# Kernel optimization log

Hardware: AMD Instinct MI355X
Metric: run time of the kernel (lower is better)

## Reference

```python
import jax, jax.numpy as jnp
import numpy as np

EPS = 1e-5

def gather_neighbour(pc, idx):
    # pc: [B,N,d], idx: [B,Q,k] -> [B,Q,k,d]
    return jax.vmap(lambda p, i: p[i])(pc, idx)

def rel_pos_encoding(q_xyz, src_xyz, idx):
    # q_xyz: [B,Q,3], src_xyz: [B,N,3], idx: [B,Q,k] -> [B,Q,k,10]
    nbr = gather_neighbour(src_xyz, idx)              # [B,Q,k,3]
    tile = q_xyz[:, :, None, :]                       # [B,Q,1,3]
    rel = tile - nbr                                  # [B,Q,k,3]
    dis = jnp.sqrt(jnp.sum(rel * rel, axis=-1, keepdims=True))
    tile_b = jnp.broadcast_to(tile, nbr.shape)
    return jnp.concatenate([dis, rel, tile_b, nbr], axis=-1)

def conv_bn_relu(x, W, g, b, m, v):
    # 1x1 conv (bias-free) + inference BatchNorm + ReLU; x: [B,Q,K,Cin], W: [Cout,Cin]
    y = jnp.einsum('bqkc,oc->bqko', x, W)
    y = (y - m) * (g * jax.lax.rsqrt(v + EPS)) + b
    return jax.nn.relu(y)

def att_pool(x, Wfc, Wm, g, b, m, v):
    # x: [B,Q,K,C] -> [B,Q,1,Cout]; softmax over neighbor axis K
    att = jnp.einsum('bqkc,oc->bqko', x, Wfc)
    att = jax.nn.softmax(att, axis=2)
    agg = jnp.sum(x * att, axis=2, keepdims=True)     # [B,Q,1,C]
    return conv_bn_relu(agg, Wm, g, b, m, v)

def setup_inputs() -> dict:
    key = jax.random.key(0)
    ks = jax.random.split(key, 40)
    B, Q, k, Nd, Ns = 2, 16384, 16, 4096, 16384
    dim_lb, dim_sc, dim_nl = 128, 64, 128
    d_mid = dim_lb + 10 - dim_sc   # 74
    d_att = dim_lb + 10            # 138
    f32 = jnp.float32
    inp = {}
    inp['features_lb'] = jax.random.normal(ks[0], (B, Q, k, dim_lb), f32)
    inp['features_sc'] = jax.random.normal(ks[1], (B, Q, k, dim_sc), f32)
    inp['NM_lb'] = jax.random.randint(ks[2], (B, Q, k), 0, Nd)
    inp['NM_sc'] = jax.random.randint(ks[3], (B, Q, k), 0, Ns)
    inp['coords_lb'] = jax.random.normal(ks[4], (B, Nd, 3), f32)
    inp['coords_sc'] = jax.random.normal(ks[5], (B, Ns, 3), f32)
    inp['coords_queries'] = jax.random.normal(ks[6], (B, Q, 3), f32)
    inp['NM_cl'] = jax.random.randint(ks[7], (B, Q, k), 0, Q)
    def bn(i, c):
        return (jax.random.uniform(ks[i], (c,), f32) + 0.5,
                jax.random.normal(ks[i + 1], (c,), f32) * 0.1,
                jax.random.normal(ks[i + 2], (c,), f32) * 0.1,
                jax.random.uniform(ks[i + 3], (c,), f32) + 0.5)
    inp['W_lb'] = jax.random.normal(ks[8], (10, 10), f32) * 0.3
    inp['g_lb'], inp['b_lb'], inp['m_lb'], inp['v_lb'] = bn(9, 10)
    inp['W_sc'] = jax.random.normal(ks[13], (d_mid, 10), f32) * 0.3
    inp['g_sc'], inp['b_sc'], inp['m_sc'], inp['v_sc'] = bn(14, d_mid)
    inp['W_fc1'] = jax.random.normal(ks[18], (d_att, d_att), f32) * 0.08
    inp['W_mlp1'] = jax.random.normal(ks[19], (dim_nl, d_att), f32) * 0.08
    inp['g1'], inp['b1'], inp['m1'], inp['v1'] = bn(20, dim_nl)
    inp['W_cl'] = jax.random.normal(ks[24], (10, 10), f32) * 0.3
    inp['g_cl'], inp['b_cl'], inp['m_cl'], inp['v_cl'] = bn(25, 10)
    inp['W_fc2'] = jax.random.normal(ks[29], (d_att, d_att), f32) * 0.08
    inp['W_mlp2'] = jax.random.normal(ks[30], (dim_nl, d_att), f32) * 0.08
    inp['g2'], inp['b2'], inp['m2'], inp['v2'] = bn(31, dim_nl)
    return inp

def reference(features_lb, features_sc, NM_lb, NM_sc, coords_lb, coords_sc,
              coords_queries, NM_cl,
              W_lb, g_lb, b_lb, m_lb, v_lb,
              W_sc, g_sc, b_sc, m_sc, v_sc,
              W_fc1, W_mlp1, g1, b1, m1, v1,
              W_cl, g_cl, b_cl, m_cl, v_cl,
              W_fc2, W_mlp2, g2, b2, m2, v2):
    # branch 1: layer-below
    rppe_lb = conv_bn_relu(rel_pos_encoding(coords_queries, coords_lb, NM_lb),
                           W_lb, g_lb, b_lb, m_lb, v_lb)          # [B,Q,k,10]
    # branch 2: skip connection
    rppe_sc = conv_bn_relu(rel_pos_encoding(coords_queries, coords_sc, NM_sc),
                           W_sc, g_sc, b_sc, m_sc, v_sc)          # [B,Q,k,74]
    locSE_lb = jnp.concatenate([rppe_lb, features_lb], axis=-1)   # [B,Q,k,138]
    locSE_sc = jnp.concatenate([rppe_sc, features_sc], axis=-1)   # [B,Q,k,138]
    f_hat = jnp.concatenate([locSE_lb, locSE_sc], axis=2)         # [B,Q,2k,138]
    f_tilde = att_pool(f_hat, W_fc1, W_mlp1, g1, b1, m1, v1)      # [B,Q,1,128]
    # second aggregation over current layer (num_agg > 1)
    rppe_cl = conv_bn_relu(rel_pos_encoding(coords_queries, coords_queries, NM_cl),
                           W_cl, g_cl, b_cl, m_cl, v_cl)          # [B,Q,k,10]
    f_cur = gather_neighbour(f_tilde[:, :, 0, :], NM_cl)          # [B,Q,k,128]
    locSE_cl = jnp.concatenate([rppe_cl, f_cur], axis=-1)         # [B,Q,k,138]
    f_tilde = att_pool(locSE_cl, W_fc2, W_mlp2, g2, b2, m2, v2)   # [B,Q,1,128]
    # match torch output layout [B, dim_nl, Q, 1]
    return jnp.transpose(f_tilde, (0, 3, 1, 2))
```

## Files before the change

### kernel.cpp

```cpp
#include <hip/hip_runtime.h>
#include <cmath>

#define EPSF 1e-5f
typedef unsigned int  uint32;
typedef unsigned short u16;
typedef __attribute__((ext_vector_type(8))) short bfrag;
typedef __attribute__((ext_vector_type(4))) float f32x4;
typedef __attribute__((ext_vector_type(16))) float f32x16;

constexpr int Qn   = 16384;
constexpr int KS   = 168;
constexpr int PXS  = 42;
constexpr int AGS  = 168;
constexpr int Nd   = 4096;
constexpr float LOG2E = 1.4426950408889634f;

constexpr int OFF_W1  = 0;
constexpr int OFF_WM1 = 23040;
constexpr int OFF_W2  = 43520;
constexpr int OFF_WM2 = 66560;
constexpr int OFF_WLB = 87040;
constexpr int OFF_WSC = 87552;
constexpr int OFF_WCL = 90112;
constexpr int END_W   = 90624;
constexpr int BN_LB = 0;
constexpr int BN_SC = 20;
constexpr int BN_CL = 168;
constexpr int BN_M1 = 188;
constexpr int BN_M2 = 444;
constexpr int BN_TOT = 700;
constexpr int OFF_FT  = END_W + 2 * BN_TOT;
constexpr int OFF_AG  = OFF_FT + 2 * Qn * 128;
constexpr int OFF_W32 = OFF_AG + 2 * Qn * AGS;
constexpr int N_W32   = 2 * 5 * 10 * 512;
constexpr int PREP_N  = END_W + BN_TOT;

__device__ __forceinline__ u16 f2b(float f) {
    uint32 u = __float_as_uint(f);
    uint32 r = (u + 0x7fffu + ((u >> 16) & 1u)) >> 16;
    return (u16)r;
}
__device__ __forceinline__ float b2f(u16 h) {
    return __uint_as_float(((uint32)h) << 16);
}
__device__ __forceinline__ uint32 cvtpk(float a, float b) {
    uint32 r;
    asm("v_cvt_pk_bf16_f32 %0, %1, %2" : "=v"(r) : "v"(a), "v"(b));
    return r;
}
__device__ __forceinline__ u16 cvt1(float a) { return (u16)cvtpk(a, a); }
__device__ __forceinline__ float exp2_hw(float x) { return __builtin_amdgcn_exp2f(x); }

__global__ __launch_bounds__(256) void prep_weights(
    const float* __restrict__ Wfc1, const float* __restrict__ Wmlp1,
    const float* __restrict__ Wfc2, const float* __restrict__ Wmlp2,
    const float* __restrict__ Wlb,  const float* __restrict__ Wsc,
    const float* __restrict__ Wcl,
    const float* __restrict__ g_lb, const float* __restrict__ b_lb,
    const float* __restrict__ m_lb, const float* __restrict__ v_lb,
    const float* __restrict__ g_sc, const float* __restrict__ b_sc,
    const float* __restrict__ m_sc, const float* __restrict__ v_sc,
    const float* __restrict__ g_cl, const float* __restrict__ b_cl,
    const float* __restrict__ m_cl, const float* __restrict__ v_cl,
    const float* __restrict__ g1, const float* __restrict__ b1,
    const float* __restrict__ m1, const float* __restrict__ v1,
    const float* __restrict__ g2, const float* __restrict__ b2,
    const float* __restrict__ m2, const float* __restrict__ v2,
    u16* __restrict__ ws16)
{
    int i = blockIdx.x * 256 + threadIdx.x;
    if (i >= PREP_N) return;
    if (i >= END_W) {
        int j = i - END_W;
        const float *g, *bb, *m, *v; int o2;
        if (j < BN_SC)      { g = g_lb; bb = b_lb; m = m_lb; v = v_lb; o2 = j - BN_LB; }
        else if (j < BN_CL) { g = g_sc; bb = b_sc; m = m_sc; v = v_sc; o2 = j - BN_SC; }
        else if (j < BN_M1) { g = g_cl; bb = b_cl; m = m_cl; v = v_cl; o2 = j - BN_CL; }
        else if (j < BN_M2) { g = g1;   bb = b1;   m = m1;   v = v1;   o2 = j - BN_M1; }
        else                { g = g2;   bb = b2;   m = m2;   v = v2;   o2 = j - BN_M2; }
        int o = o2 >> 1;
        float sc_ = g[o] * rsqrtf(v[o] + EPSF);
        ((float*)(ws16 + END_W))[j] = (o2 & 1) ? (bb[o] - m[o] * sc_) : sc_;
        return;
    }
    int lane = (i >> 3) & 63, jj = i & 7;
    int row16 = lane & 15;
    int kf = ((lane >> 4) << 3) + jj;
    float v = 0.f;
    if (i < OFF_WLB) {
        const float* src; int nrows; int idx; bool fc = false;
        if (i < OFF_WM1)      { src = Wfc1;  nrows = 138; idx = i - OFF_W1;  fc = true; }
        else if (i < OFF_W2)  { src = Wmlp1; nrows = 128; idx = i - OFF_WM1; }
        else if (i < OFF_WM2) { src = Wfc2;  nrows = 138; idx = i - OFF_W2;  fc = true; }
        else                  { src = Wmlp2; nrows = 128; idx = i - OFF_WM2; }
        int t = idx >> 9, nt = t / 5, kt = t - nt * 5;
        int row = nt * 16 + row16;
        int kp  = kt * 32 + kf;
        int k   = (kp < 10) ? kp : kp - 2;
        if (row < nrows && kp < 140 && kp != 10 && kp != 11) {
            v = src[row * 138 + k];
            if (fc) v *= LOG2E;
        }
    } else {
        const float* src; int nrows; int idx;
        if (i < OFF_WSC)      { src = Wlb; nrows = 10; idx = i - OFF_WLB; }
        else if (i < OFF_WCL) { src = Wsc; nrows = 74; idx = i - OFF_WSC; }
        else                  { src = Wcl; nrows = 10; idx = i - OFF_WCL; }
        int t = idx >> 9;
        int row = t * 16 + row16;
        if (row < nrows && kf < 10) v = src[row * 10 + kf];
    }
    ws16[i] = f2b(v);
}

__global__ __launch_bounds__(256) void prep_weights32(
    const float* __restrict__ Wfc1, const float* __restrict__ Wfc2,
    u16* __restrict__ ws16)
{
    int i = blockIdx.x * 256 + threadIdx.x;
    if (i >= N_W32) return;
    const float* src = (i < N_W32 / 2) ? Wfc1 : Wfc2;
    int idx = (i < N_W32 / 2) ? i : i - N_W32 / 2;
    int t = idx >> 9;
    int lane = (idx >> 3) & 63, j = idx & 7;
    int nt = t / 10, kt = t - nt * 10;
    int o  = nt * 32 + (lane & 31);
    int kp = kt * 16 + ((lane >> 5) << 3) + j;
    int k  = (kp < 10) ? kp : kp - 2;
    float v = 0.f;
    if (o < 138 && kp < 140 && kp != 10 && kp != 11) v = src[o * 138 + k] * LOG2E;
    ws16[OFF_W32 + i] = f2b(v);
}

__device__ __forceinline__ void loadB(bfrag (&bf)[5], const u16* __restrict__ Wt,
                                      int nt, int lane) {
    #pragma unroll
    for (int kt = 0; kt < 5; ++kt)
        bf[kt] = *(const bfrag*)&Wt[((nt * 5 + kt) << 9) + (lane << 3)];
}
__device__ __forceinline__ void mfma16(const bfrag (&af)[5], const bfrag (&bf)[5],
                                       f32x4 &a0) {
    const f32x4 zf = {0.f, 0.f, 0.f, 0.f};
    a0 = zf;
    #pragma unroll
    for (int kt = 0; kt < 5; ++kt)
        a0 = __builtin_amdgcn_mfma_f32_16x16x32_bf16(af[kt], bf[kt], a0, 0, 0, 0);
}
__device__ __forceinline__ void soft16(
    const f32x4& a0, int nt,
    int lane, int lrow, const u16* __restrict__ fr0, u16* __restrict__ ag)
{
    const int ch  = nt * 16 + lrow;
    const int chp = ch + (ch >= 10 ? 2 : 0);
    float s = 0.f, num = 0.f;
    #pragma unroll
    for (int r = 0; r < 4; ++r) {
        float e = exp2_hw(a0[r]);
        s += e;
        num += e * b2f(fr0[r * KS + chp]);
    }
    s   += __shfl_xor(s, 16);   s   += __shfl_xor(s, 32);
    num += __shfl_xor(num, 16); num += __shfl_xor(num, 32);
    if (lane < 16)
        ag[chp] = cvt1((ch < 138) ? num * __builtin_amdgcn_rcpf(s) : 0.f);
}
#define SB() __builtin_amdgcn_sched_barrier(0)

__device__ __forceinline__ void unit32(
    int nt, const bfrag (&af32)[10], const u16* __restrict__ W32,
    int lane, const u16* __restrict__ frh, u16* __restrict__ ag)
{
    f32x16 acc;
    #pragma unroll
    for (int r = 0; r < 16; ++r) acc[r] = 0.f;
    #pragma unroll
    for (int kt = 0; kt < 10; ++kt) {
        bfrag bf = *(const bfrag*)&W32[((nt * 10 + kt) << 9) + (lane << 3)];
        acc = __builtin_amdgcn_mfma_f32_32x32x16_bf16(af32[kt], bf, acc, 0, 0, 0);
    }
    const int ch  = nt * 32 + (lane & 31);
    const int chp = ch + (ch >= 10 ? 2 : 0);
    float s = 0.f, num = 0.f;
    #pragma unroll
    for (int reg = 0; reg < 16; ++reg) {
        float e = exp2_hw(acc[reg]);
        s += e;
        const int brow = (reg & 3) + 8 * (reg >> 2);
        num += e * b2f(frh[brow * KS + chp]);
    }
    s   += __shfl_xor(s, 32);
    num += __shfl_xor(num, 32);
    if (lane < 32)
        ag[chp] = cvt1((ch < 138) ? num * __builtin_amdgcn_rcpf(s) : 0.f);
}

__global__ __launch_bounds__(128, 8) void stage1(
    const float* __restrict__ feat_lb, const float* __restrict__ feat_sc,
    const int* __restrict__ nm_lb, const int* __restrict__ nm_sc,
    const float* __restrict__ c_lb, const float* __restrict__ c_sc,
    const float* __restrict__ c_q,
    u16* __restrict__ ws16)
{
    __shared__ __align__(16) u16 fhat[32 * KS];
    __shared__ __align__(16) u16 pxs[32 * PXS];

    const int tid  = threadIdx.x;
    const int bq   = blockIdx.x;
    const int b    = bq >> 14;
    const int lane = tid & 63;
    const int h    = tid >> 6;
    const int lrow = lane & 15;
    const int lgr  = lane >> 4;

    const u16* W32  = ws16 + OFF_W32;
    const float* bn = (const float*)(ws16 + END_W);
    u16* ag = ws16 + OFF_AG + (size_t)bq * AGS;

    bfrag wcv[3];
    float2 bnv[3];
    if (h == 0) {
        wcv[0] = *(const bfrag*)&ws16[OFF_WLB + (lane << 3)];
        wcv[1] = *(const bfrag*)&ws16[OFF_WSC + (lane << 3)];
        wcv[2] = *(const bfrag*)&ws16[OFF_WSC + 512 + (lane << 3)];
        bnv[0] = (lrow < 10) ? *(const float2*)&bn[BN_LB + lrow * 2] : float2{0.f, 0.f};
        bnv[1] = *(const float2*)&bn[BN_SC + lrow * 2];
        bnv[2] = *(const float2*)&bn[BN_SC + (16 + lrow) * 2];
    } else {
        #pragma unroll
        for (int t = 0; t < 3; ++t) {
            wcv[t] = *(const bfrag*)&ws16[OFF_WSC + ((2 + t) << 9) + (lane << 3)];
            int o = (2 + t) * 16 + lrow;
            bnv[t] = (o < 74) ? *(const float2*)&bn[BN_SC + o * 2] : float2{0.f, 0.f};
        }
    }

    {
        const float4* flb = (const float4*)(feat_lb + (size_t)bq * 2048);
        float4 r0[4];
        #pragma unroll
        for (int it = 0; it < 4; ++it) r0[it] = flb[tid + it * 128];
        const float4* fsc = (const float4*)(feat_sc + (size_t)bq * 1024);
        float4 r1[2];
        #pragma unroll
        for (int it = 0; it < 2; ++it) r1[it] = fsc[tid + it * 128];
        #pragma unroll
        for (int it = 0; it < 4; ++it) {
            int u = tid + it * 128;
            int nbr = u >> 5, c4 = u & 31;
            uint32* d = (uint32*)&fhat[nbr * KS + 12 + c4 * 4];
            d[0] = cvtpk(r0[it].x, r0[it].y); d[1] = cvtpk(r0[it].z, r0[it].w);
        }
        #pragma unroll
        for (int it = 0; it < 2; ++it) {
            int u = tid + it * 128;
            int nbr = u >> 4, c4 = u & 15;
            uint32* d = (uint32*)&fhat[(16 + nbr) * KS + 76 + c4 * 4];
            d[0] = cvtpk(r1[it].x, r1[it].y); d[1] = cvtpk(r1[it].z, r1[it].w);
        }
        if (tid < 32) ((uint32*)((char*)fhat + tid * 336))[5] = 0u;
        #pragma unroll
        for (int it = 0; it < 4; ++it) {
            int u = tid + it * 128;
            if (u < 448) {
                int row = u / 14, jj = u - row * 14;
                ((uint32*)((char*)fhat + row * 336))[70 + jj] = 0u;
            }
        }
    }
    if (tid < 32) {
        const int r = tid;
        const bool lb = r < 16;
        const int idx = lb ? nm_lb[bq * 16 + r] : nm_sc[bq * 16 + (r - 16)];
        const float* nb = lb ? (c_lb + ((size_t)b * Nd + idx) * 3)
                             : (c_sc + ((size_t)b * Qn + idx) * 3);
        const float qx = c_q[bq * 3 + 0], qy = c_q[bq * 3 + 1], qz = c_q[bq * 3 + 2];
        const float nx = nb[0], ny = nb[1], nz = nb[2];
        const float rx = qx - nx, ry = qy - ny, rz = qz - nz;
        const float dd = sqrtf(rx * rx + ry * ry + rz * rz);
        uint32* pw = (uint32*)&pxs[tid * PXS];
        pw[0] = cvtpk(dd, rx); pw[1] = cvtpk(ry, rz); pw[2] = cvtpk(qx, qy);
        pw[3] = cvtpk(qz, nx); pw[4] = cvtpk(ny, nz);
        #pragma unroll
        for (int z = 5; z < 16; ++z) pw[z] = 0u;
    }
    __syncthreads();

    const f32x4 zf = {0.f, 0.f, 0.f, 0.f};

    {
        bfrag pa1 = *(const bfrag*)&pxs[(16 + lrow) * PXS + lgr * 8];
        if (h == 0) {
            bfrag pa0 = *(const bfrag*)&pxs[lrow * PXS + lgr * 8];
            f32x4 c = __builtin_amdgcn_mfma_f32_16x16x32_bf16(pa0, wcv[0], zf, 0, 0, 0);
            if (lrow < 10) {
                #pragma unroll
                for (int r = 0; r < 4; ++r)
                    fhat[(lgr * 4 + r) * KS + lrow] =
                        cvt1(fmaxf(c[r] * bnv[0].x + bnv[0].y, 0.f));
            }
            #pragma unroll
            for (int t = 1; t < 3; ++t) {
                f32x4 c2 = __builtin_amdgcn_mfma_f32_16x16x32_bf16(pa1, wcv[t], zf, 0, 0, 0);
                const int o  = (t - 1) * 16 + lrow;
                const int cp = (o < 10) ? o : o + 2;
                #pragma unroll
                for (int r = 0; r < 4; ++r)
                    fhat[(16 + lgr * 4 + r) * KS + cp] =
                        cvt1(fmaxf(c2[r] * bnv[t].x + bnv[t].y, 0.f));
            }
        } else {
            #pragma unroll
            for (int t = 0; t < 3; ++t) {
                f32x4 c2 = __builtin_amdgcn_mfma_f32_16x16x32_bf16(pa1, wcv[t], zf, 0, 0, 0);
                const int o = (2 + t) * 16 + lrow;
                if (o < 74) {
                    #pragma unroll
                    for (int r = 0; r < 4; ++r)
                        fhat[(16 + lgr * 4 + r) * KS + o + 2] =
                            cvt1(fmaxf(c2[r] * bnv[t].x + bnv[t].y, 0.f));
                }
            }
        }
    }
    __syncthreads();

    bfrag af32[10];
    #pragma unroll
    for (int kt = 0; kt < 10; ++kt)
        af32[kt] = *(const bfrag*)&fhat[(lane & 31) * KS + kt * 16 + ((lane >> 5) << 3)];
    const u16* frh = fhat + (lane >> 5) * 4 * KS;

    if (h == 0) {
        unit32(0, af32, W32, lane, frh, ag);
        unit32(1, af32, W32, lane, frh, ag);
        unit32(2, af32, W32, lane, frh, ag);
        if (lane < 2) ag[10 + lane] = 0;
    } else {
        unit32(3, af32, W32, lane, frh, ag);
        unit32(4, af32, W32, lane, frh, ag);
    }
}

__global__ __launch_bounds__(256) void mlp1(const u16* __restrict__ ws16,
                                            u16* __restrict__ ws16w)
{
    const int tid  = threadIdx.x;
    const int lane = tid & 63;
    const int w    = tid >> 6;
    const int lrow = lane & 15;
    const int lgr  = lane >> 4;
    const int q0   = (blockIdx.x * 4 + w) * 16;

    const u16* Wm = ws16 + OFF_WM1;
    const float* bn = (const float*)(ws16 + END_W);
    const u16* agg = ws16 + OFF_AG;
    u16* ftg = ws16w + OFF_FT;

    bfrag af[5];
    #pragma unroll
    for (int kt = 0; kt < 5; ++kt)
        af[kt] = *(const bfrag*)&agg[(size_t)(q0 + lrow) * AGS + kt * 32 + lgr * 8];

    const f32x4 zf = {0.f, 0.f, 0.f, 0.f};
    #pragma unroll
    for (int ot = 0; ot < 8; ++ot) {
        bfrag bf[5];
        loadB(bf, Wm, ot, lane);
        f32x4 c = zf;
        #pragma unroll
        for (int kt = 0; kt < 5; ++kt)
            c = __builtin_amdgcn_mfma_f32_16x16x32_bf16(af[kt], bf[kt], c, 0, 0, 0);
        const int o = ot * 16 + lrow;
        float2 p = *(const float2*)&bn[BN_M1 + o * 2];
        #pragma unroll
        for (int r = 0; r < 4; ++r) {
            int q = q0 + lgr * 4 + r;
            ftg[(size_t)q * 128 + o] = cvt1(fmaxf(c[r] * p.x + p.y, 0.f));
        }
    }
}

__global__ __launch_bounds__(512, 4) void stage2(
    const int* __restrict__ nm_cl, const float* __restrict__ c_q,
    const u16* __restrict__ ws16, float* __restrict__ out)
{
    __shared__ __align__(16) u16 fhat[128 * KS];
    __shared__ __align__(16) u16 pxs[128 * PXS];
    u16* aggs = pxs;

    const int tid  = threadIdx.x;
    const int bq0  = blockIdx.x * 8;
    const int b    = bq0 >> 14;
    const int q0   = bq0 & (Qn - 1);
    const int lane = tid & 63;
    const int w    = tid >> 6;
    const int lrow = lane & 15;
    const int lgr  = lane >> 4;

    const u16* W2t  = ws16 + OFF_W2;
    const u16* Wm2t = ws16 + OFF_WM2;
    const float* bn = (const float*)(ws16 + END_W);
    const u16* ft   = ws16 + OFF_FT;

    bfrag wcl = *(const bfrag*)&ws16[OFF_WCL + (lane << 3)];
    float2 bncl = (lrow < 10) ? *(const float2*)&bn[BN_CL + lrow * 2] : float2{0.f, 0.f};

    for (int u = tid; u < 128 * 15; u += 512) {
        int row = u / 15, jj = u - row * 15;
        uint32* base = (uint32*)((char*)fhat + row * 336);
        if (jj == 0) base[5] = 0u; else base[69 + jj] = 0u;
    }
    if (tid < 128) {
        const int qq = tid >> 4, r = tid & 15;
        const int bq = bq0 + qq;
        const int idx = nm_cl[bq * 16 + r];
        const float* nb = c_q + ((size_t)(b << 14) + idx) * 3;
        const float qx = c_q[bq * 3 + 0], qy = c_q[bq * 3 + 1], qz = c_q[bq * 3 + 2];
        const float nx = nb[0], ny = nb[1], nz = nb[2];
        const float rx = qx - nx, ry = qy - ny, rz = qz - nz;
        const float dd = sqrtf(rx * rx + ry * ry + rz * rz);
        uint32* pw = (uint32*)&pxs[tid * PXS];
        pw[0] = cvtpk(dd, rx); pw[1] = cvtpk(ry, rz); pw[2] = cvtpk(qx, qy);
        pw[3] = cvtpk(qz, nx); pw[4] = cvtpk(ny, nz);
        #pragma unroll
        for (int z = 5; z < 16; ++z) pw[z] = 0u;
    }
    #pragma unroll
    for (int i = 0; i < 16; ++i) {
        int u = tid + i * 512;
        int row = u >> 6, c2 = u & 63;
        int qq = row >> 4;
        int idx = nm_cl[(bq0 + qq) * 16 + (row & 15)];
        const uint32* srow = (const uint32*)(ft + (size_t)((b << 14) + idx) * 128);
        *(uint32*)&fhat[row * KS + 12 + c2 * 2] = srow[c2];
    }
    __syncthreads();

    const f32x4 zf = {0.f, 0.f, 0.f, 0.f};

    {
        bfrag pa = *(const bfrag*)&pxs[(w * 16 + lrow) * PXS + lgr * 8];
        f32x4 c = __builtin_amdgcn_mfma_f32_16x16x32_bf16(pa, wcl, zf, 0, 0, 0);
        if (lrow < 10) {
            #pragma unroll
            for (int r = 0; r < 4; ++r)
                fhat[(w * 16 + lgr * 4 + r) * KS + lrow] =
                    cvt1(fmaxf(c[r] * bncl.x + bncl.y, 0.f));
        }
    }
    __syncthreads();

    bfrag af[5];
    #pragma unroll
    for (int kt = 0; kt < 5; ++kt)
        af[kt] = *(const bfrag*)&fhat[(w * 16 + lrow) * KS + kt * 32 + lgr * 8];

    const u16* fr0 = fhat + (w * 16 + lgr * 4) * KS;
    u16* ag = aggs + w * AGS;

    bfrag b0[5], b1[5];
    f32x4 a0;
    loadB(b0, W2t, 0, lane);
    loadB(b1, W2t, 1, lane); mfma16(af, b0, a0); SB(); soft16(a0, 0, lane, lrow, fr0, ag);
    loadB(b0, W2t, 2, lane); mfma16(af, b1, a0); SB(); soft16(a0, 1, lane, lrow, fr0, ag);
    loadB(b1, W2t, 3, lane); mfma16(af, b0, a0); SB(); soft16(a0, 2, lane, lrow, fr0, ag);
    loadB(b0, W2t, 4, lane); mfma16(af, b1, a0); SB(); soft16(a0, 3, lane, lrow, fr0, ag);
    loadB(b1, W2t, 5, lane); mfma16(af, b0, a0); SB(); soft16(a0, 4, lane, lrow, fr0, ag);
    loadB(b0, W2t, 6, lane); mfma16(af, b1, a0); SB(); soft16(a0, 5, lane, lrow, fr0, ag);
    loadB(b1, W2t, 7, lane); mfma16(af, b0, a0); SB(); soft16(a0, 6, lane, lrow, fr0, ag);
    loadB(b0, W2t, 8, lane); mfma16(af, b1, a0); SB(); soft16(a0, 7, lane, lrow, fr0, ag);
    mfma16(af, b0, a0); soft16(a0, 8, lane, lrow, fr0, ag);
    if (lane < 2)       ag[10 + lane] = 0;
    else if (lane < 16) ag[144 + lane] = 0;
    __syncthreads();

    bfrag am[5];
    #pragma unroll
    for (int kt = 0; kt < 5; ++kt)
        am[kt] = *(const bfrag*)&aggs[lrow * AGS + kt * 32 + lgr * 8];
    {
        f32x4 c = zf;
        #pragma unroll
        for (int kt = 0; kt < 5; ++kt) {
            bfrag wm = *(const bfrag*)&Wm2t[(((w * 5) + kt) << 9) + (lane << 3)];
            c = __builtin_amdgcn_mfma_f32_16x16x32_bf16(am[kt], wm, c, 0, 0, 0);
        }
        if (lgr < 2) {
            const int o = w * 16 + lrow;
            float2 p = *(const float2*)&bn[BN_M2 + o * 2];
            #pragma unroll
            for (int r = 0; r < 4; ++r) {
                const int qloc = lgr * 4 + r;
                out[((size_t)(b * 128 + o) << 14) + q0 + qloc] = fmaxf(c[r] * p.x + p.y, 0.f);
            }
        }
    }
}

extern "C" void kernel_launch(void* const* d_in, const int* in_sizes, int n_in,
                              void* d_out, int out_size, void* d_ws, size_t ws_size,
                              hipStream_t stream)
{
    const float* feat_lb = (const float*)d_in[0];
    const float* feat_sc = (const float*)d_in[1];
    const int*   nm_lb   = (const int*)d_in[2];
    const int*   nm_sc   = (const int*)d_in[3];
    const float* c_lb    = (const float*)d_in[4];
    const float* c_sc    = (const float*)d_in[5];
    const float* c_q     = (const float*)d_in[6];
    const int*   nm_cl   = (const int*)d_in[7];
    const float* W_lb = (const float*)d_in[8];
    const float* g_lb = (const float*)d_in[9];
    const float* b_lb = (const float*)d_in[10];
    const float* m_lb = (const float*)d_in[11];
    const float* v_lb = (const float*)d_in[12];
    const float* W_sc = (const float*)d_in[13];
    const float* g_sc = (const float*)d_in[14];
    const float* b_sc = (const float*)d_in[15];
    const float* m_sc = (const float*)d_in[16];
    const float* v_sc = (const float*)d_in[17];
    const float* W_fc1  = (const float*)d_in[18];
    const float* W_mlp1 = (const float*)d_in[19];
    const float* g1 = (const float*)d_in[20];
    const float* b1 = (const float*)d_in[21];
    const float* m1 = (const float*)d_in[22];
    const float* v1 = (const float*)d_in[23];
    const float* W_cl = (const float*)d_in[24];
    const float* g_cl = (const float*)d_in[25];
    const float* b_cl = (const float*)d_in[26];
    const float* m_cl = (const float*)d_in[27];
    const float* v_cl = (const float*)d_in[28];
    const float* W_fc2  = (const float*)d_in[29];
    const float* W_mlp2 = (const float*)d_in[30];
    const float* g2 = (const float*)d_in[31];
    const float* b2 = (const float*)d_in[32];
    const float* m2 = (const float*)d_in[33];
    const float* v2 = (const float*)d_in[34];

    u16* ws16 = (u16*)d_ws;
    float* out = (float*)d_out;

    hipLaunchKernelGGL(prep_weights, dim3((PREP_N + 255) / 256), dim3(256), 0, stream,
        W_fc1, W_mlp1, W_fc2, W_mlp2, W_lb, W_sc, W_cl,
        g_lb, b_lb, m_lb, v_lb, g_sc, b_sc, m_sc, v_sc,
        g_cl, b_cl, m_cl, v_cl, g1, b1, m1, v1, g2, b2, m2, v2, ws16);

    hipLaunchKernelGGL(prep_weights32, dim3((N_W32 + 255) / 256), dim3(256), 0, stream,
        W_fc1, W_fc2, ws16);

    hipLaunchKernelGGL(stage1, dim3(2 * Qn), dim3(128), 0, stream,
        feat_lb, feat_sc, nm_lb, nm_sc, c_lb, c_sc, c_q, ws16);

    hipLaunchKernelGGL(mlp1, dim3(2 * Qn / 64), dim3(256), 0, stream, ws16, ws16);

    hipLaunchKernelGGL(stage2, dim3(2 * Qn / 8), dim3(512), 0, stream,
        nm_cl, c_q, ws16, out);
}
```

Before: 229.4 us.

## Switch stage1 attention scoring from 32x32 MFMA tiles back to 16x16 tiles

The attention-score matmul in stage1 now uses 16x16x32 bf16 MFMAs over two 16-row halves, with double-buffered B-fragment loads from the existing 16x16 weight layout, instead of 32x32x16 MFMAs. This removes the separate prep_weights32 kernel launch and its extra 32x32 weight layout. Scheduling barriers separate each MFMA batch from its softmax. The cost is more MFMA instructions and more per-channel-tile softmax passes (9 vs 5 units), and padding channels 144-159 are explicitly zeroed.

```diff
diff --git a/kernel.cpp b/kernel.cpp
--- a/kernel.cpp
+++ b/kernel.cpp
@@ -6,7 +6,6 @@
 typedef unsigned short u16;
 typedef __attribute__((ext_vector_type(8))) short bfrag;
 typedef __attribute__((ext_vector_type(4))) float f32x4;
-typedef __attribute__((ext_vector_type(16))) float f32x16;
 
 constexpr int Qn   = 16384;
 constexpr int KS   = 168;
@@ -31,8 +30,6 @@
 constexpr int BN_TOT = 700;
 constexpr int OFF_FT  = END_W + 2 * BN_TOT;
 constexpr int OFF_AG  = OFF_FT + 2 * Qn * 128;
-constexpr int OFF_W32 = OFF_AG + 2 * Qn * AGS;
-constexpr int N_W32   = 2 * 5 * 10 * 512;
 constexpr int PREP_N  = END_W + BN_TOT;
 
 __device__ __forceinline__ u16 f2b(float f) {
@@ -113,30 +110,21 @@
     ws16[i] = f2b(v);
 }
 
-__global__ __launch_bounds__(256) void prep_weights32(
-    const float* __restrict__ Wfc1, const float* __restrict__ Wfc2,
-    u16* __restrict__ ws16)
-{
-    int i = blockIdx.x * 256 + threadIdx.x;
-    if (i >= N_W32) return;
-    const float* src = (i < N_W32 / 2) ? Wfc1 : Wfc2;
-    int idx = (i < N_W32 / 2) ? i : i - N_W32 / 2;
-    int t = idx >> 9;
-    int lane = (idx >> 3) & 63, j = idx & 7;
-    int nt = t / 10, kt = t - nt * 10;
-    int o  = nt * 32 + (lane & 31);
-    int kp = kt * 16 + ((lane >> 5) << 3) + j;
-    int k  = (kp < 10) ? kp : kp - 2;
-    float v = 0.f;
-    if (o < 138 && kp < 140 && kp != 10 && kp != 11) v = src[o * 138 + k] * LOG2E;
-    ws16[OFF_W32 + i] = f2b(v);
-}
-
 __device__ __forceinline__ void loadB(bfrag (&bf)[5], const u16* __restrict__ Wt,
                                       int nt, int lane) {
     #pragma unroll
     for (int kt = 0; kt < 5; ++kt)
         bf[kt] = *(const bfrag*)&Wt[((nt * 5 + kt) << 9) + (lane << 3)];
+}
+__device__ __forceinline__ void mfma32(const bfrag (&af)[2][5], const bfrag (&bf)[5],
+                                       f32x4 &a0, f32x4 &a1) {
+    const f32x4 zf = {0.f, 0.f, 0.f, 0.f};
+    a0 = zf; a1 = zf;
+    #pragma unroll
+    for (int kt = 0; kt < 5; ++kt) {
+        a0 = __builtin_amdgcn_mfma_f32_16x16x32_bf16(af[0][kt], bf[kt], a0, 0, 0, 0);
+        a1 = __builtin_amdgcn_mfma_f32_16x16x32_bf16(af[1][kt], bf[kt], a1, 0, 0, 0);
+    }
 }
 __device__ __forceinline__ void mfma16(const bfrag (&af)[5], const bfrag (&bf)[5],
                                        f32x4 &a0) {
@@ -146,9 +134,10 @@
     for (int kt = 0; kt < 5; ++kt)
         a0 = __builtin_amdgcn_mfma_f32_16x16x32_bf16(af[kt], bf[kt], a0, 0, 0, 0);
 }
-__device__ __forceinline__ void soft16(
-    const f32x4& a0, int nt,
-    int lane, int lrow, const u16* __restrict__ fr0, u16* __restrict__ ag)
+__device__ __forceinline__ void soft32(
+    const f32x4& a0, const f32x4& a1, int nt,
+    int lane, int lrow, const u16* __restrict__ fr0, const u16* __restrict__ fr1,
+    u16* __restrict__ ag)
 {
     const int ch  = nt * 16 + lrow;
     const int chp = ch + (ch >= 10 ? 2 : 0);
@@ -159,40 +148,36 @@
         s += e;
         num += e * b2f(fr0[r * KS + chp]);
     }
+    #pragma unroll
+    for (int r = 0; r < 4; ++r) {
+        float e = exp2_hw(a1[r]);
+        s += e;
+        num += e * b2f(fr1[r * KS + chp]);
+    }
     s   += __shfl_xor(s, 16);   s   += __shfl_xor(s, 32);
     num += __shfl_xor(num, 16); num += __shfl_xor(num, 32);
     if (lane < 16)
         ag[chp] = cvt1((ch < 138) ? num * __builtin_amdgcn_rcpf(s) : 0.f);
 }
-#define SB() __builtin_amdgcn_sched_barrier(0)
-
-__device__ __forceinline__ void unit32(
-    int nt, const bfrag (&af32)[10], const u16* __restrict__ W32,
-    int lane, const u16* __restrict__ frh, u16* __restrict__ ag)
-{
-    f32x16 acc;
-    #pragma unroll
-    for (int r = 0; r < 16; ++r) acc[r] = 0.f;
-    #pragma unroll
-    for (int kt = 0; kt < 10; ++kt) {
-        bfrag bf = *(const bfrag*)&W32[((nt * 10 + kt) << 9) + (lane << 3)];
-        acc = __builtin_amdgcn_mfma_f32_32x32x16_bf16(af32[kt], bf, acc, 0, 0, 0);
-    }
-    const int ch  = nt * 32 + (lane & 31);
+__device__ __forceinline__ void soft16(
+    const f32x4& a0, int nt,
+    int lane, int lrow, const u16* __restrict__ fr0, u16* __restrict__ ag)
+{
+    const int ch  = nt * 16 + lrow;
     const int chp = ch + (ch >= 10 ? 2 : 0);
     float s = 0.f, num = 0.f;
     #pragma unroll
-    for (int reg = 0; reg < 16; ++reg) {
-        float e = exp2_hw(acc[reg]);
+    for (int r = 0; r < 4; ++r) {
+        float e = exp2_hw(a0[r]);
         s += e;
-        const int brow = (reg & 3) + 8 * (reg >> 2);
-        num += e * b2f(frh[brow * KS + chp]);
-    }
-    s   += __shfl_xor(s, 32);
-    num += __shfl_xor(num, 32);
-    if (lane < 32)
+        num += e * b2f(fr0[r * KS + chp]);
+    }
+    s   += __shfl_xor(s, 16);   s   += __shfl_xor(s, 32);
+    num += __shfl_xor(num, 16); num += __shfl_xor(num, 32);
+    if (lane < 16)
         ag[chp] = cvt1((ch < 138) ? num * __builtin_amdgcn_rcpf(s) : 0.f);
 }
+#define SB() __builtin_amdgcn_sched_barrier(0)
 
 __global__ __launch_bounds__(128, 8) void stage1(
     const float* __restrict__ feat_lb, const float* __restrict__ feat_sc,
@@ -212,7 +197,7 @@
     const int lrow = lane & 15;
     const int lgr  = lane >> 4;
 
-    const u16* W32  = ws16 + OFF_W32;
+    const u16* W1t  = ws16 + OFF_W1;
     const float* bn = (const float*)(ws16 + END_W);
     u16* ag = ws16 + OFF_AG + (size_t)bq * AGS;
 
@@ -324,20 +309,33 @@
     }
     __syncthreads();
 
-    bfrag af32[10];
-    #pragma unroll
-    for (int kt = 0; kt < 10; ++kt)
-        af32[kt] = *(const bfrag*)&fhat[(lane & 31) * KS + kt * 16 + ((lane >> 5) << 3)];
-    const u16* frh = fhat + (lane >> 5) * 4 * KS;
-
+    bfrag af[2][5];
+    #pragma unroll
+    for (int mt = 0; mt < 2; ++mt)
+        #pragma unroll
+        for (int kt = 0; kt < 5; ++kt)
+            af[mt][kt] = *(const bfrag*)&fhat[(mt * 16 + lrow) * KS + kt * 32 + lgr * 8];
+
+    const u16* fr0 = fhat + (lgr * 4) * KS;
+    const u16* fr1 = fr0 + 16 * KS;
+
+    bfrag b0[5], b1[5];
+    f32x4 a0, a1;
     if (h == 0) {
-        unit32(0, af32, W32, lane, frh, ag);
-        unit32(1, af32, W32, lane, frh, ag);
-        unit32(2, af32, W32, lane, frh, ag);
-        if (lane < 2) ag[10 + lane] = 0;
+        loadB(b0, W1t, 0, lane);
+        loadB(b1, W1t, 1, lane); mfma32(af, b0, a0, a1); SB(); soft32(a0, a1, 0, lane, lrow, fr0, fr1, ag);
+        loadB(b0, W1t, 2, lane); mfma32(af, b1, a0, a1); SB(); soft32(a0, a1, 1, lane, lrow, fr0, fr1, ag);
+        loadB(b1, W1t, 3, lane); mfma32(af, b0, a0, a1); SB(); soft32(a0, a1, 2, lane, lrow, fr0, fr1, ag);
+        loadB(b0, W1t, 4, lane); mfma32(af, b1, a0, a1); SB(); soft32(a0, a1, 3, lane, lrow, fr0, fr1, ag);
+        mfma32(af, b0, a0, a1); soft32(a0, a1, 4, lane, lrow, fr0, fr1, ag);
+        if (lane < 2)       ag[10 + lane] = 0;
+        else if (lane < 16) ag[144 + lane] = 0;
     } else {
-        unit32(3, af32, W32, lane, frh, ag);
-        unit32(4, af32, W32, lane, frh, ag);
+        loadB(b0, W1t, 5, lane);
+        loadB(b1, W1t, 6, lane); mfma32(af, b0, a0, a1); SB(); soft32(a0, a1, 5, lane, lrow, fr0, fr1, ag);
+        loadB(b0, W1t, 7, lane); mfma32(af, b1, a0, a1); SB(); soft32(a0, a1, 6, lane, lrow, fr0, fr1, ag);
+        loadB(b1, W1t, 8, lane); mfma32(af, b0, a0, a1); SB(); soft32(a0, a1, 7, lane, lrow, fr0, fr1, ag);
+        mfma32(af, b1, a0, a1); soft32(a0, a1, 8, lane, lrow, fr0, fr1, ag);
     }
 }
 
@@ -545,9 +543,6 @@
         g_lb, b_lb, m_lb, v_lb, g_sc, b_sc, m_sc, v_sc,
         g_cl, b_cl, m_cl, v_cl, g1, b1, m1, v1, g2, b2, m2, v2, ws16);
 
-    hipLaunchKernelGGL(prep_weights32, dim3((N_W32 + 255) / 256), dim3(256), 0, stream,
-        W_fc1, W_fc2, ws16);
-
     hipLaunchKernelGGL(stage1, dim3(2 * Qn), dim3(128), 0, stream,
         feat_lb, feat_sc, nm_lb, nm_sc, c_lb, c_sc, c_q, ws16);
 
```

Result: faster. 219.7 us (-4.2%).
